# Kernel optimization log

Hardware: AMD Instinct MI355X
Metric: run time of the kernel (lower is better)

The kernel has to match this reference:

```python
import math
import jax, jax.numpy as jnp
import numpy as np

B, T, D = 8, 2048, 512
EPS = 1e-5


def _gate(x, W, b, a, g, beta):
    # Linear -> PReLU (single shared slope a) -> LayerNorm -> sigmoid
    h = x @ W.T + b
    h = jnp.where(h >= 0, h, a * h)
    mu = jnp.mean(h, axis=-1, keepdims=True)
    var = jnp.var(h, axis=-1, keepdims=True)
    h = (h - mu) / jnp.sqrt(var + EPS) * g + beta
    return jax.nn.sigmoid(h)


def setup_inputs() -> dict:
    key = jax.random.key(0)
    ks = jax.random.split(key, 12)
    lin = lambda k: jax.random.normal(k, (D, D), jnp.float32) * 0.02
    z = jnp.zeros((D,), jnp.float32)
    o = jnp.ones((D,), jnp.float32)
    a0 = jnp.float32(0.25)  # PReLU default init
    inp = {
        "query": jax.random.normal(ks[0], (B, T, D), jnp.float32),
        "value": jax.random.normal(ks[1], (B, T, D), jnp.float32),
        "aux_emb": jax.random.normal(ks[2], (B, 1, D), jnp.float32),
        # ragged valid lengths in [T//2, T] to keep every sample realistic
        "input_len": jax.random.randint(ks[3], (B,), T // 2, T + 1),
        "Wq": lin(ks[4]), "bq": z,
        "Wqg": lin(ks[5]), "bqg": z, "aq": a0, "gq": o, "betaq": z,
        "Wkg": lin(ks[6]), "bkg": z, "ak": a0, "gk": o, "betak": z,
        "Wvg": lin(ks[7]), "bvg": z, "av": a0, "gv": o, "betav": z,
        "Wsig": lin(ks[8]), "bsig": z,
        "Wtan": lin(ks[9]), "btan": z,
    }
    return inp


def reference(query, value, aux_emb, input_len,
              Wq, bq,
              Wqg, bqg, aq, gq, betaq,
              Wkg, bkg, ak, gk, betak,
              Wvg, bvg, av, gv, betav,
              Wsig, bsig, Wtan, btan):
    q = query @ Wq.T + bq
    q = q * _gate(aux_emb, Wqg, bqg, aq, gq, betaq)          # [B,T,D]
    k = value * _gate(aux_emb, Wkg, bkg, ak, gk, betak)      # [B,T,D]
    vg = _gate(aux_emb, Wvg, bvg, av, gv, betav)             # [B,1,D]
    vg = jax.nn.sigmoid(vg @ Wsig.T + bsig) * jnp.tanh(vg @ Wtan.T + btan)
    v = value * vg                                           # [B,T,D]

    w = jnp.einsum('btd,bsd->bts', q, k) / math.sqrt(D)      # [B,T,T]
    r = jnp.arange(T)
    causal = (r[:, None] >= r[None, :]).astype(w.dtype)      # tril ones
    w = w * causal
    w = jnp.where(w == 0.0, -jnp.inf, w)  # torch quirk: exact zeros -> -inf
    L = input_len[:, None, None]                              # [B,1,1]
    invalid = (r[None, :, None] < L) & (r[None, None, :] >= L)
    w = jnp.where(invalid, -jnp.inf, w)
    p = jax.nn.softmax(w, axis=-1)
    # rows beyond input_len are padding: zero them (torch code produced NaN
    # there via -inf*0; intended semantics is zeroed padding rows)
    row_valid = (r[None, :, None] < L).astype(p.dtype)        # [B,T,1]
    p = p * row_valid
    return p @ v                                              # [B,T,D]
```

## Files before the change

### kernel.cpp

```cpp
#include <hip/hip_runtime.h>
#include <hip/hip_bf16.h>
#include <stdint.h>

#define BB 8
#define TT 2048
#define DD 512

typedef __attribute__((ext_vector_type(8))) __bf16 bf16x8;
typedef __attribute__((ext_vector_type(4))) float f32x4;
typedef __attribute__((ext_vector_type(8))) unsigned short ushort8_t;

__device__ __forceinline__ unsigned short f2bf(float f) {
    unsigned u = __builtin_bit_cast(unsigned, f);
    unsigned r = u + 0x7fffu + ((u >> 16) & 1u);
    return (unsigned short)(r >> 16);
}

__device__ __forceinline__ void gload_lds16(const unsigned short* g, unsigned short* l) {
    __builtin_amdgcn_global_load_lds(
        (const __attribute__((address_space(1))) void*)g,
        (__attribute__((address_space(3))) void*)l, 16, 0, 0);
}

__global__ __launch_bounds__(256) void gates_mv1(
    const float* __restrict__ aux,
    const float* __restrict__ Wqg, const float* __restrict__ bqg, const float* __restrict__ aq,
    const float* __restrict__ Wkg, const float* __restrict__ bkg, const float* __restrict__ ak,
    const float* __restrict__ Wvg, const float* __restrict__ bvg, const float* __restrict__ av,
    float* __restrict__ h) {
    __shared__ float saux[BB * DD];
    int tid = threadIdx.x;
#pragma unroll
    for (int i = 0; i < 4; i++) {
        int idx = tid + i * 256;
        ((float4*)saux)[idx] = ((const float4*)aux)[idx];
    }
    __syncthreads();
    int wave = (blockIdx.x * 256 + tid) >> 6;
    int lane = tid & 63;
    int g = wave >> 9, r = wave & 511;
    const float* W    = (g == 0) ? Wqg : (g == 1) ? Wkg : Wvg;
    const float* bias = (g == 0) ? bqg : (g == 1) ? bkg : bvg;
    const float* alpha = (g == 0) ? aq : (g == 1) ? ak : av;
    const float4* Wrow = (const float4*)(W + (size_t)r * DD);
    float acc[BB];
#pragma unroll
    for (int b = 0; b < BB; b++) acc[b] = 0.f;
#pragma unroll
    for (int c = 0; c < 2; c++) {
        float4 w4 = Wrow[lane + c * 64];
#pragma unroll
        for (int b = 0; b < BB; b++) {
            float4 a4 = ((const float4*)(saux + b * DD))[lane + c * 64];
            acc[b] += w4.x * a4.x + w4.y * a4.y + w4.z * a4.z + w4.w * a4.w;
        }
    }
#pragma unroll
    for (int b = 0; b < BB; b++) {
#pragma unroll
        for (int s = 1; s < 64; s <<= 1) acc[b] += __shfl_xor(acc[b], s, 64);
    }
    if (lane == 0) {
        float bi = bias[r], a = alpha[0];
#pragma unroll
        for (int b = 0; b < BB; b++) {
            float v = acc[b] + bi;
            v = (v >= 0.f) ? v : a * v;
            h[(g * BB + b) * DD + r] = v;
        }
    }
}

__global__ __launch_bounds__(512) void gates_norm(
    const float* __restrict__ h,
    const float* __restrict__ gq, const float* __restrict__ betaq,
    const float* __restrict__ gk, const float* __restrict__ betak,
    const float* __restrict__ gv, const float* __restrict__ betav,
    float* __restrict__ qgate, float* __restrict__ kgate, float* __restrict__ vg) {
    int g = blockIdx.x >> 3, b = blockIdx.x & 7, tid = threadIdx.x;
    __shared__ float red[DD], red2[DD];
    float hv = h[(g * BB + b) * DD + tid];
    red[tid] = hv; red2[tid] = hv * hv;
    __syncthreads();
    for (int s = 256; s > 0; s >>= 1) {
        if (tid < s) { red[tid] += red[tid + s]; red2[tid] += red2[tid + s]; }
        __syncthreads();
    }
    float mu = red[0] * (1.f / DD);
    float var = red2[0] * (1.f / DD) - mu * mu;
    const float* gg = (g == 0) ? gq : (g == 1) ? gk : gv;
    const float* be = (g == 0) ? betaq : (g == 1) ? betak : betav;
    float val = (hv - mu) * rsqrtf(var + 1e-5f) * gg[tid] + be[tid];
    float sg = 1.f / (1.f + expf(-val));
    float* outp = (g == 0) ? qgate : (g == 1) ? kgate : vg;
    outp[b * DD + tid] = sg;
}

__global__ __launch_bounds__(256) void gates_mv2(
    const float* __restrict__ vg,
    const float* __restrict__ Wsig, const float* __restrict__ bsig,
    const float* __restrict__ Wtan, const float* __restrict__ btan,
    float* __restrict__ vgate) {
    __shared__ float svg[BB * DD];
    int tid = threadIdx.x;
#pragma unroll
    for (int i = 0; i < 4; i++) {
        int idx = tid + i * 256;
        ((float4*)svg)[idx] = ((const float4*)vg)[idx];
    }
    __syncthreads();
    int r = (blockIdx.x * 256 + tid) >> 6;
    int lane = tid & 63;
    const float4* Ws = (const float4*)(Wsig + (size_t)r * DD);
    const float4* Wt = (const float4*)(Wtan + (size_t)r * DD);
    float as_[BB], at_[BB];
#pragma unroll
    for (int b = 0; b < BB; b++) { as_[b] = 0.f; at_[b] = 0.f; }
#pragma unroll
    for (int c = 0; c < 2; c++) {
        float4 w1 = Ws[lane + c * 64];
        float4 w2 = Wt[lane + c * 64];
#pragma unroll
        for (int b = 0; b < BB; b++) {
            float4 a4 = ((const float4*)(svg + b * DD))[lane + c * 64];
            as_[b] += w1.x * a4.x + w1.y * a4.y + w1.z * a4.z + w1.w * a4.w;
            at_[b] += w2.x * a4.x + w2.y * a4.y + w2.z * a4.z + w2.w * a4.w;
        }
    }
#pragma unroll
    for (int b = 0; b < BB; b++) {
#pragma unroll
        for (int s = 1; s < 64; s <<= 1) {
            as_[b] += __shfl_xor(as_[b], s, 64);
            at_[b] += __shfl_xor(at_[b], s, 64);
        }
    }
    if (lane == 0) {
        float b1 = bsig[r], b2 = btan[r];
#pragma unroll
        for (int b = 0; b < BB; b++) {
            float s1 = 1.f / (1.f + expf(-(as_[b] + b1)));
            float s2 = tanhf(at_[b] + b2);
            vgate[b * DD + r] = s1 * s2;
        }
    }
}

__global__ __launch_bounds__(256) void convert_kernel(
    const float* __restrict__ query, const float* __restrict__ Wq,
    const float* __restrict__ value,
    const float* __restrict__ kgate, const float* __restrict__ vgate,
    unsigned short* __restrict__ queryb, unsigned short* __restrict__ Wqb,
    unsigned short* __restrict__ kb, unsigned short* __restrict__ vbT) {
    __shared__ float tileF[64][65];
    int bi = blockIdx.x, tid = threadIdx.x;
    if (bi < 8192) {
        int idx = bi * 256 + tid;
        float4 q4 = ((const float4*)query)[idx];
        ushort4 oq;
        oq.x = f2bf(q4.x); oq.y = f2bf(q4.y); oq.z = f2bf(q4.z); oq.w = f2bf(q4.w);
        ((ushort4*)queryb)[idx] = oq;
    } else if (bi < 8448) {
        int idx = (bi - 8192) * 256 + tid;
        float4 w4 = ((const float4*)Wq)[idx];
        ushort4 o;
        o.x = f2bf(w4.x); o.y = f2bf(w4.y); o.z = f2bf(w4.z); o.w = f2bf(w4.w);
        ((ushort4*)Wqb)[idx] = o;
    } else {
        int vb = bi - 8448;
        int tIdx = vb & 31, dIdx = (vb >> 5) & 7, b = vb >> 8;
        int t0 = tIdx * 64, d0 = dIdx * 64;
        int row = tid >> 2;
        int cg = tid & 3;
        float v[16], kgv[16];
        const float* src = &value[((size_t)b * TT + t0 + row) * DD + d0 + cg * 16];
#pragma unroll
        for (int j = 0; j < 4; j++) {
            float4 f = ((const float4*)src)[j];
            v[j * 4 + 0] = f.x; v[j * 4 + 1] = f.y; v[j * 4 + 2] = f.z; v[j * 4 + 3] = f.w;
            float4 g = *(const float4*)&kgate[b * DD + d0 + cg * 16 + j * 4];
            kgv[j * 4 + 0] = g.x; kgv[j * 4 + 1] = g.y; kgv[j * 4 + 2] = g.z; kgv[j * 4 + 3] = g.w;
        }
        ushort8_t kb8[2];
#pragma unroll
        for (int h = 0; h < 2; h++)
#pragma unroll
            for (int j = 0; j < 8; j++)
                kb8[h][j] = f2bf(v[h * 8 + j] * kgv[h * 8 + j]);
        unsigned short* kdst = &kb[((size_t)b * TT + t0 + row) * DD + d0 + cg * 16];
        *(ushort8_t*)&kdst[0] = kb8[0];
        *(ushort8_t*)&kdst[8] = kb8[1];
#pragma unroll
        for (int j = 0; j < 16; j++) tileF[row][cg * 16 + j] = v[j];
        __syncthreads();
        int d = row;
        float g = vgate[b * DD + d0 + d];
        ushort8_t o8[2];
#pragma unroll
        for (int h = 0; h < 2; h++)
#pragma unroll
            for (int j = 0; j < 8; j++)
                o8[h][j] = f2bf(tileF[cg * 16 + h * 8 + j][d] * g);
        unsigned short* vdst = &vbT[((size_t)b * DD + d0 + d) * TT + t0 + cg * 16];
        *(ushort8_t*)&vdst[0] = o8[0];
        *(ushort8_t*)&vdst[8] = o8[1];
    }
}

#define STAGE_AB(BUF, K0)                                                                 \
    _Pragma("unroll") for (int i = 0; i < 2; i++) {                                       \
        int idx = tid * 8 + i * 2048;                                                     \
        int r = idx >> 5;                                                                 \
        int cg = ((idx >> 3) & 3) ^ ((r >> 1) & 3);                                       \
        gload_lds16(&Ap_[(size_t)r * lda_ + (K0) + cg * 8], &As[BUF][idx]);               \
        gload_lds16(&Bp_[(size_t)r * ldb_ + (K0) + cg * 8], &Bs[BUF][idx]);               \
    }

#define GEMM_CORE(APTR, ALDA, BPTR, BLDA, KSTART, KEND)                                   \
    __shared__ __align__(16) unsigned short As[2][128 * 32];                              \
    __shared__ __align__(16) unsigned short Bs[2][128 * 32];                              \
    const unsigned short* Ap_ = (APTR);                                                   \
    const unsigned short* Bp_ = (BPTR);                                                   \
    const int lda_ = (ALDA), ldb_ = (BLDA);                                               \
    int tid = threadIdx.x;                                                                \
    int lane = tid & 63, wid = tid >> 6;                                                  \
    int wm = (wid >> 1) * 64, wn = (wid & 1) * 64;                                        \
    int lm = lane & 15, quad = lane >> 4;                                                 \
    f32x4 acc[4][4];                                                                      \
    _Pragma("unroll") for (int im = 0; im < 4; im++)                                      \
        _Pragma("unroll") for (int in = 0; in < 4; in++)                                  \
            acc[im][in] = (f32x4){0.f, 0.f, 0.f, 0.f};                                    \
    STAGE_AB(0, (KSTART))                                                                 \
    int cur_ = 0;                                                                         \
    for (int k0 = (KSTART); k0 < (KEND); k0 += 32) {                                      \
        __syncthreads();                                                                  \
        if (k0 + 32 < (KEND)) { STAGE_AB(cur_ ^ 1, k0 + 32) }                             \
        bf16x8 af[4], bf_[4];                                                             \
        _Pragma("unroll") for (int i = 0; i < 4; i++) {                                   \
            int row = wm + i * 16 + lm;                                                   \
            af[i] = *(const bf16x8*)&As[cur_][row * 32 + (quad ^ ((row >> 1) & 3)) * 8];  \
        }                                                                                 \
        _Pragma("unroll") for (int i = 0; i < 4; i++) {                                   \
            int row = wn + i * 16 + lm;                                                   \
            bf_[i] = *(const bf16x8*)&Bs[cur_][row * 32 + (quad ^ ((row >> 1) & 3)) * 8]; \
        }                                                                                 \
        _Pragma("unroll") for (int im = 0; im < 4; im++)                                  \
            _Pragma("unroll") for (int in = 0; in < 4; in++)                              \
                acc[im][in] = __builtin_amdgcn_mfma_f32_16x16x32_bf16(af[im], bf_[in],    \
                                                                     acc[im][in], 0, 0, 0);\
        cur_ ^= 1;                                                                        \
    }

__global__ __launch_bounds__(256) void qgemm_kernel(
    const unsigned short* __restrict__ Amat, const unsigned short* __restrict__ Bmat,
    const float* __restrict__ bq, const float* __restrict__ qgate,
    unsigned short* __restrict__ qb) {
    int m0 = blockIdx.x * 128, n0 = blockIdx.y * 128;
    const unsigned short* Ap = Amat + (size_t)m0 * DD;
    const unsigned short* Bp = Bmat + (size_t)n0 * DD;
    GEMM_CORE(Ap, DD, Bp, DD, 0, DD)
    int b = m0 >> 11;
#pragma unroll
    for (int im = 0; im < 4; im++) {
        int row = m0 + wm + im * 16 + quad * 4;
#pragma unroll
        for (int in = 0; in < 4; in++) {
            int col = n0 + wn + in * 16 + lm;
            float bias = bq[col];
            float g = qgate[b * DD + col];
#pragma unroll
            for (int r = 0; r < 4; r++) {
                float v = (acc[im][in][r] + bias) * g;
                qb[(size_t)(row + r) * DD + col] = f2bf(v);
            }
        }
    }
}

__global__ __launch_bounds__(256) void scores_kernel(
    const unsigned short* __restrict__ qb, const unsigned short* __restrict__ kb,
    unsigned short* __restrict__ P, float* __restrict__ rowsum) {
    int lin = blockIdx.x + 136 * blockIdx.z;
    int b = lin & 7;
    int idx = lin >> 3;
    int mt = (int)((sqrtf(8.f * idx + 1.f) - 1.f) * 0.5f);
    while ((mt + 1) * (mt + 2) / 2 <= idx) mt++;
    while (mt * (mt + 1) / 2 > idx) mt--;
    int nt = idx - mt * (mt + 1) / 2;
    int t0 = mt * 128, s0 = nt * 128;
    const unsigned short* Ap = qb + ((size_t)b * TT + t0) * DD;
    const unsigned short* Bp = kb + ((size_t)b * TT + s0) * DD;
    GEMM_CORE(Ap, DD, Bp, DD, 0, DD)
    const float scale = 0.044194173824159216f;
    unsigned short* Ptile = P + ((size_t)b * 136 + (size_t)mt * (mt + 1) / 2 + nt) * 16384;
#pragma unroll
    for (int im = 0; im < 4; im++) {
        int ltb = wm + im * 16 + quad * 4;
        float rs[4] = {0.f, 0.f, 0.f, 0.f};
#pragma unroll
        for (int in = 0; in < 4; in++) {
            int ls = wn + in * 16 + lm;
            int s = s0 + ls;
#pragma unroll
            for (int r = 0; r < 4; r++) {
                float p = (s <= t0 + ltb + r) ? expf(acc[im][in][r] * scale) : 0.f;
                Ptile[(size_t)(ltb + r) * 128 + ls] = f2bf(p);
                rs[r] += p;
            }
        }
#pragma unroll
        for (int r = 0; r < 4; r++) {
            float v = rs[r];
            v += __shfl_xor(v, 1, 64);
            v += __shfl_xor(v, 2, 64);
            v += __shfl_xor(v, 4, 64);
            v += __shfl_xor(v, 8, 64);
            if (lm == 0) atomicAdd(&rowsum[b * TT + t0 + ltb + r], v);
        }
    }
}

__global__ __launch_bounds__(256) void out_kernel(
    const unsigned short* __restrict__ P, const unsigned short* __restrict__ vbT,
    const float* __restrict__ rowsum, const int* __restrict__ input_len,
    float* __restrict__ out) {
    int lin = blockIdx.x + 4 * blockIdx.y + 64 * blockIdx.z;
    int b = lin & 7;
    int rem = lin >> 3;
    int nt = rem & 3;
    int pr = rem >> 2;
    int n0 = nt * 128;
    int L = input_len[b];

    __shared__ __align__(16) unsigned short As[2][64 * 64];
    __shared__ __align__(16) unsigned short Bs[2][128 * 64];
    int tid = threadIdx.x;
    int lane = tid & 63, wid = tid >> 6;
    int wm = (wid >> 1) * 32, wn = (wid & 1) * 64;
    int lm = lane & 15, quad = lane >> 4;

#pragma unroll
    for (int half = 0; half < 2; half++) {
        int mt = half ? (31 - pr) : pr;
        int t0 = mt * 64;
        int mt128 = mt >> 1;
        int rowoff = (mt & 1) * 64;
        size_t triBase = ((size_t)b * 136 + (size_t)mt128 * (mt128 + 1) / 2) * 16384;
        int ksteps = mt + 1;

        f32x4 acc[2][4];
#pragma unroll
        for (int im = 0; im < 2; im++)
#pragma unroll
            for (int in = 0; in < 4; in++) acc[im][in] = (f32x4){0.f, 0.f, 0.f, 0.f};

#define OUT_STAGE(BUF, KS)                                                              \
        {                                                                               \
            int k0s = (KS) * 64;                                                        \
            int stile = k0s >> 7;                                                       \
            int coloff = k0s & 64;                                                      \
            _Pragma("unroll") for (int i = 0; i < 2; i++) {                             \
                int idx = tid * 8 + i * 2048;                                           \
                int r = idx >> 6;                                                       \
                int c = (idx >> 3) & 7;                                                 \
                int cs = c ^ (r & 7);                                                   \
                const unsigned short* ag = P + triBase + (size_t)stile * 16384 +        \
                                           (size_t)(rowoff + r) * 128 + coloff + cs * 8;\
                gload_lds16(ag, &As[BUF][idx]);                                         \
            }                                                                           \
            _Pragma("unroll") for (int i = 0; i < 4; i++) {                             \
                int idx = tid * 8 + i * 2048;                                           \
                int r = idx >> 6;                                                       \
                int c = (idx >> 3) & 7;                                                 \
                int cs = c ^ (r & 7);                                                   \
                gload_lds16(&vbT[(size_t)(b * DD + n0 + r) * TT + k0s + cs * 8],        \
                            &Bs[BUF][idx]);                                             \
            }                                                                           \
        }

        OUT_STAGE(0, 0)
        int cur = 0;
        for (int ks = 0; ks < ksteps; ks++) {
            __syncthreads();
            if (ks + 1 < ksteps) { OUT_STAGE(cur ^ 1, ks + 1) }
            bf16x8 af[2][2], bf_[4][2];
#pragma unroll
            for (int kk = 0; kk < 2; kk++) {
#pragma unroll
                for (int i = 0; i < 2; i++) {
                    int row = wm + i * 16 + lm;
                    af[i][kk] = *(const bf16x8*)&As[cur][row * 64 + ((kk * 4 + quad) ^ (row & 7)) * 8];
                }
#pragma unroll
                for (int i = 0; i < 4; i++) {
                    int row = wn + i * 16 + lm;
                    bf_[i][kk] = *(const bf16x8*)&Bs[cur][row * 64 + ((kk * 4 + quad) ^ (row & 7)) * 8];
                }
            }
#pragma unroll
            for (int kk = 0; kk < 2; kk++)
#pragma unroll
                for (int im = 0; im < 2; im++)
#pragma unroll
                    for (int in = 0; in < 4; in++)
                        acc[im][in] = __builtin_amdgcn_mfma_f32_16x16x32_bf16(
                            af[im][kk], bf_[in][kk], acc[im][in], 0, 0, 0);
            cur ^= 1;
        }
        __syncthreads();
#undef OUT_STAGE

#pragma unroll
        for (int im = 0; im < 2; im++) {
            int tbase = t0 + wm + im * 16 + quad * 4;
#pragma unroll
            for (int r = 0; r < 4; r++) {
                int t = tbase + r;
                float inv = 1.f / rowsum[b * TT + t];
                bool valid = (t < L);
#pragma unroll
                for (int in = 0; in < 4; in++) {
                    int n = n0 + wn + in * 16 + lm;
                    float o = valid ? acc[im][in][r] * inv : 0.f;
                    out[((size_t)b * TT + t) * DD + n] = o;
                }
            }
        }
    }
}

extern "C" void kernel_launch(void* const* d_in, const int* in_sizes, int n_in,
                              void* d_out, int out_size, void* d_ws, size_t ws_size,
                              hipStream_t stream) {
    const float* query = (const float*)d_in[0];
    const float* value = (const float*)d_in[1];
    const float* aux   = (const float*)d_in[2];
    const int*   ilen  = (const int*)d_in[3];
    const float* Wq    = (const float*)d_in[4];
    const float* bq    = (const float*)d_in[5];
    const float* Wqg   = (const float*)d_in[6];
    const float* bqg   = (const float*)d_in[7];
    const float* aq    = (const float*)d_in[8];
    const float* gq    = (const float*)d_in[9];
    const float* betaq = (const float*)d_in[10];
    const float* Wkg   = (const float*)d_in[11];
    const float* bkg   = (const float*)d_in[12];
    const float* ak    = (const float*)d_in[13];
    const float* gk    = (const float*)d_in[14];
    const float* betak = (const float*)d_in[15];
    const float* Wvg   = (const float*)d_in[16];
    const float* bvg   = (const float*)d_in[17];
    const float* av    = (const float*)d_in[18];
    const float* gv    = (const float*)d_in[19];
    const float* betav = (const float*)d_in[20];
    const float* Wsig  = (const float*)d_in[21];
    const float* bsig  = (const float*)d_in[22];
    const float* Wtan  = (const float*)d_in[23];
    const float* btan  = (const float*)d_in[24];

    char* ws = (char*)d_ws;
    float* qgate          = (float*)(ws + 0);
    float* kgate          = (float*)(ws + 16384);
    float* vgate          = (float*)(ws + 32768);
    float* rowsum         = (float*)(ws + 49152);
    unsigned short* Wqb   = (unsigned short*)(ws + 114688);
    unsigned short* queryb= (unsigned short*)(ws + 638976);
    unsigned short* qb    = (unsigned short*)(ws + 17416192);
    unsigned short* kb    = (unsigned short*)(ws + 34193408);
    unsigned short* vbT   = (unsigned short*)(ws + 50970624);
    unsigned short* P     = (unsigned short*)(ws + 67747840);
    float* hbuf           = (float*)(ws + 67747840);
    float* vg             = (float*)(ws + 67747840 + 49152);

    hipMemsetAsync(rowsum, 0, BB * TT * sizeof(float), stream);

    gates_mv1<<<384, 256, 0, stream>>>(aux, Wqg, bqg, aq, Wkg, bkg, ak, Wvg, bvg, av, hbuf);
    gates_norm<<<24, 512, 0, stream>>>(hbuf, gq, betaq, gk, betak, gv, betav,
                                       qgate, kgate, vg);
    gates_mv2<<<128, 256, 0, stream>>>(vg, Wsig, bsig, Wtan, btan, vgate);

    convert_kernel<<<10496, 256, 0, stream>>>(query, Wq, value, kgate, vgate,
                                              queryb, Wqb, kb, vbT);
    qgemm_kernel<<<dim3((BB * TT) / 128, DD / 128), 256, 0, stream>>>(queryb, Wqb, bq, qgate, qb);
    scores_kernel<<<dim3(136, 1, BB), 256, 0, stream>>>(qb, kb, P, rowsum);
    out_kernel<<<dim3(4, 16, BB), 256, 0, stream>>>(P, vbT, rowsum, ilen, (float*)d_out);
}
```

Baseline: 259.5 us.

## Triple-buffer LDS staging with explicit vmcnt waits in GEMM kernels

Both the shared GEMM core and the output kernel move from double to triple buffering of LDS tiles. Loads are issued two stages ahead, and the block synchronisation becomes explicit s_waitcnt vmcnt counts plus s_barrier, so more global-to-LDS traffic can be in flight while MFMAs run. The block-index mapping is also simplified to use the grid dimensions directly, replacing the batch-interleaved linearisation, and the half loop is no longer unrolled. In exchange LDS use grows, which may reduce occupancy, and the hand-counted vmcnt values must match the exact number of loads each stage issues.

```diff
diff --git a/kernel.cpp b/kernel.cpp
--- a/kernel.cpp
+++ b/kernel.cpp
@@ -217,8 +217,8 @@
     }
 
 #define GEMM_CORE(APTR, ALDA, BPTR, BLDA, KSTART, KEND)                                   \
-    __shared__ __align__(16) unsigned short As[2][128 * 32];                              \
-    __shared__ __align__(16) unsigned short Bs[2][128 * 32];                              \
+    __shared__ __align__(16) unsigned short As[3][128 * 32];                              \
+    __shared__ __align__(16) unsigned short Bs[3][128 * 32];                              \
     const unsigned short* Ap_ = (APTR);                                                   \
     const unsigned short* Bp_ = (BPTR);                                                   \
     const int lda_ = (ALDA), ldb_ = (BLDA);                                               \
@@ -231,10 +231,16 @@
         _Pragma("unroll") for (int in = 0; in < 4; in++)                                  \
             acc[im][in] = (f32x4){0.f, 0.f, 0.f, 0.f};                                    \
     STAGE_AB(0, (KSTART))                                                                 \
+    if ((KSTART) + 32 < (KEND)) { STAGE_AB(1, (KSTART) + 32) }                            \
+    if ((KSTART) + 64 < (KEND)) { STAGE_AB(2, (KSTART) + 64) }                            \
     int cur_ = 0;                                                                         \
     for (int k0 = (KSTART); k0 < (KEND); k0 += 32) {                                      \
-        __syncthreads();                                                                  \
-        if (k0 + 32 < (KEND)) { STAGE_AB(cur_ ^ 1, k0 + 32) }                             \
+        int rem_ = ((KEND) - k0 - 32) >> 5;                                               \
+        if (rem_ >= 2)      { asm volatile("s_waitcnt vmcnt(8)" ::: "memory"); }          \
+        else if (rem_ == 1) { asm volatile("s_waitcnt vmcnt(4)" ::: "memory"); }          \
+        else                { asm volatile("s_waitcnt vmcnt(0)" ::: "memory"); }          \
+        __builtin_amdgcn_s_barrier();                                                     \
+        __builtin_amdgcn_sched_barrier(0);                                                \
         bf16x8 af[4], bf_[4];                                                             \
         _Pragma("unroll") for (int i = 0; i < 4; i++) {                                   \
             int row = wm + i * 16 + lm;                                                   \
@@ -248,7 +254,10 @@
             _Pragma("unroll") for (int in = 0; in < 4; in++)                              \
                 acc[im][in] = __builtin_amdgcn_mfma_f32_16x16x32_bf16(af[im], bf_[in],    \
                                                                      acc[im][in], 0, 0, 0);\
-        cur_ ^= 1;                                                                        \
+        __builtin_amdgcn_sched_barrier(0);                                                \
+        __builtin_amdgcn_s_barrier();                                                     \
+        if (k0 + 96 < (KEND)) { STAGE_AB(cur_, k0 + 96) }                                 \
+        cur_ = (cur_ == 2) ? 0 : cur_ + 1;                                                \
     }
 
 __global__ __launch_bounds__(256) void qgemm_kernel(
@@ -280,9 +289,8 @@
 __global__ __launch_bounds__(256) void scores_kernel(
     const unsigned short* __restrict__ qb, const unsigned short* __restrict__ kb,
     unsigned short* __restrict__ P, float* __restrict__ rowsum) {
-    int lin = blockIdx.x + 136 * blockIdx.z;
-    int b = lin & 7;
-    int idx = lin >> 3;
+    int b = blockIdx.z;
+    int idx = blockIdx.x;
     int mt = (int)((sqrtf(8.f * idx + 1.f) - 1.f) * 0.5f);
     while ((mt + 1) * (mt + 2) / 2 <= idx) mt++;
     while (mt * (mt + 1) / 2 > idx) mt--;
@@ -324,22 +332,20 @@
     const unsigned short* __restrict__ P, const unsigned short* __restrict__ vbT,
     const float* __restrict__ rowsum, const int* __restrict__ input_len,
     float* __restrict__ out) {
-    int lin = blockIdx.x + 4 * blockIdx.y + 64 * blockIdx.z;
-    int b = lin & 7;
-    int rem = lin >> 3;
-    int nt = rem & 3;
-    int pr = rem >> 2;
+    int nt = blockIdx.x;
+    int pr = blockIdx.y;
+    int b = blockIdx.z;
     int n0 = nt * 128;
     int L = input_len[b];
 
-    __shared__ __align__(16) unsigned short As[2][64 * 64];
-    __shared__ __align__(16) unsigned short Bs[2][128 * 64];
+    __shared__ __align__(16) unsigned short As[3][64 * 64];
+    __shared__ __align__(16) unsigned short Bs[3][128 * 64];
     int tid = threadIdx.x;
     int lane = tid & 63, wid = tid >> 6;
     int wm = (wid >> 1) * 32, wn = (wid & 1) * 64;
     int lm = lane & 15, quad = lane >> 4;
 
-#pragma unroll
+#pragma unroll 1
     for (int half = 0; half < 2; half++) {
         int mt = half ? (31 - pr) : pr;
         int t0 = mt * 64;
@@ -379,10 +385,16 @@
         }
 
         OUT_STAGE(0, 0)
+        if (1 < ksteps) { OUT_STAGE(1, 1) }
+        if (2 < ksteps) { OUT_STAGE(2, 2) }
         int cur = 0;
         for (int ks = 0; ks < ksteps; ks++) {
-            __syncthreads();
-            if (ks + 1 < ksteps) { OUT_STAGE(cur ^ 1, ks + 1) }
+            int rem = ksteps - ks - 1;
+            if (rem >= 2)      { asm volatile("s_waitcnt vmcnt(12)" ::: "memory"); }
+            else if (rem == 1) { asm volatile("s_waitcnt vmcnt(6)" ::: "memory"); }
+            else               { asm volatile("s_waitcnt vmcnt(0)" ::: "memory"); }
+            __builtin_amdgcn_s_barrier();
+            __builtin_amdgcn_sched_barrier(0);
             bf16x8 af[2][2], bf_[4][2];
 #pragma unroll
             for (int kk = 0; kk < 2; kk++) {
@@ -405,9 +417,11 @@
                     for (int in = 0; in < 4; in++)
                         acc[im][in] = __builtin_amdgcn_mfma_f32_16x16x32_bf16(
                             af[im][kk], bf_[in][kk], acc[im][in], 0, 0, 0);
-            cur ^= 1;
-        }
-        __syncthreads();
+            __builtin_amdgcn_sched_barrier(0);
+            __builtin_amdgcn_s_barrier();
+            if (ks + 3 < ksteps) { OUT_STAGE(cur, ks + 3) }
+            cur = (cur == 2) ? 0 : cur + 1;
+        }
 #undef OUT_STAGE
 
 #pragma unroll
```

Result: slower. 272.1 us (+4.9%).
